# Kernel tuning notes

Hardware: AMD Instinct MI355X
Metric: run time of the kernel (lower is better)

## Reference

```python
import jax, jax.numpy as jnp
import numpy as np

NUM_CLASSES = 5
SMOOTH = 1e-5


def setup_inputs() -> dict:
    key = jax.random.key(0)
    k1, k2, k3 = jax.random.split(key, 3)
    B, C, X, Y, Z = 2, NUM_CLASSES, 128, 128, 128
    net_output = jax.random.normal(k1, (B, C, X, Y, Z), dtype=jnp.float32)
    target = jax.random.randint(k2, (B, 1, X, Y, Z), 0, C, dtype=jnp.int64)
    dist = jax.random.uniform(k3, (B, 1, X, Y, Z), dtype=jnp.float32)
    return {"net_output": net_output, "target": target, "dist": dist}


def reference(net_output, target, dist):
    # --- Distance-map penalized multi-class Dice ---
    p = jax.nn.softmax(net_output, axis=1)  # (B,C,X,Y,Z)
    gt = target[:, 0]  # (B,X,Y,Z)
    classes = jnp.arange(NUM_CLASSES)[None, :, None, None, None]
    y_onehot = (gt[:, None] == classes).astype(p.dtype)  # (B,C,X,Y,Z)
    # per-class, per-batch sums over spatial dims
    tp = jnp.sum(p * y_onehot * dist, axis=(2, 3, 4))  # (B,C), dist broadcasts over C
    denom = jnp.sum(p, axis=(2, 3, 4)) + jnp.sum(y_onehot, axis=(2, 3, 4))  # (B,C)
    dc = (2.0 * tp + SMOOTH) / (denom + SMOOTH)  # (B,C)
    # sum over classes of batch-mean, divided by num_classes == overall mean
    dpdc_loss = -jnp.mean(dc)
    # --- Cross entropy (mean over all voxels), target squeezed to class idx ---
    logp = jax.nn.log_softmax(net_output, axis=1)  # (B,C,X,Y,Z)
    nll = -jnp.take_along_axis(logp, target, axis=1)  # (B,1,X,Y,Z)
    ce_loss = jnp.mean(nll)
    # aggregate == 'sum', weight_ce = weight_dice = 1
    return ce_loss + dpdc_loss
```

## Files before the change

### kernel.cpp

```cpp
#include <hip/hip_runtime.h>

#define NC 5
#define NB 2
#define SPATIAL (128*128*128)
#define NVEC (SPATIAL/4)
#define SMOOTHF 1e-5f
#define NREP 32
#define GRIDX 1024
#define ITERS (NVEC / (GRIDX * 256))


__global__ __launch_bounds__(1024) void init_and_detect(
    const unsigned long long* __restrict__ t, float* __restrict__ acc) {
    acc[threadIdx.x] = 0.f;
    if (threadIdx.x == 0) {
        int is64 = 1;
        for (int i = 0; i < 64; ++i)
            if (t[i] >= 5ull) { is64 = 0; break; }
        ((int*)acc)[NREP * 32] = is64;
    }
}

__global__ __launch_bounds__(256) void dpdc_main(
    const float* __restrict__ net, const void* __restrict__ targ,
    const float* __restrict__ dist, float* __restrict__ acc)
{
    const int b = blockIdx.y;
    const int t64 = ((const int*)acc)[NREP * 32];
    const float4* nb = (const float4*)(net + (size_t)b * NC * SPATIAL);
    const float4* db = (const float4*)(dist + (size_t)b * SPATIAL);
    const int4* t32p = (const int4*)((const int*)targ + (size_t)b * SPATIAL);
    const ulonglong2* t64p =
        (const ulonglong2*)((const unsigned long long*)targ + (size_t)b * SPATIAL);

    float tp[NC] = {0,0,0,0,0}, sp[NC] = {0,0,0,0,0}, cnt[NC] = {0,0,0,0,0};
    float nll = 0.f;

    int i = blockIdx.x * blockDim.x + threadIdx.x;
    const int stride = GRIDX * 256;
    #pragma unroll
    for (int it = 0; it < ITERS; ++it, i += stride) {
        float4 l[NC];
        #pragma unroll
        for (int c = 0; c < NC; ++c) l[c] = nb[(size_t)c * NVEC + i];
        float4 dd = db[i];
        int tt[4];
        if (t64) {
            ulonglong2 a = t64p[2 * i];
            ulonglong2 bq = t64p[2 * i + 1];
            tt[0] = (int)a.x; tt[1] = (int)a.y;
            tt[2] = (int)bq.x; tt[3] = (int)bq.y;
        } else {
            int4 a = t32p[i];
            tt[0] = a.x; tt[1] = a.y; tt[2] = a.z; tt[3] = a.w;
        }
        const float* dv = (const float*)&dd;
        #pragma unroll
        for (int j = 0; j < 4; ++j) {
            float lc[NC];
            #pragma unroll
            for (int c = 0; c < NC; ++c) lc[c] = ((const float*)&l[c])[j];
            float m = fmaxf(fmaxf(fmaxf(lc[0], lc[1]), fmaxf(lc[2], lc[3])), lc[4]);
            float e[NC];
            float s = 0.f;
            #pragma unroll
            for (int c = 0; c < NC; ++c) { e[c] = __expf(lc[c] - m); s += e[c]; }
            float inv = 1.0f / s;
            int t = tt[j];
            float lsel = lc[4];
            #pragma unroll
            for (int c = 0; c < 4; ++c) lsel = (t == c) ? lc[c] : lsel;
            float pd = dv[j] * inv;
            #pragma unroll
            for (int c = 0; c < NC; ++c) {
                float p = e[c] * inv;
                sp[c] += p;
                tp[c] += (t == c) ? e[c] * pd : 0.f;
                cnt[c] += (t == c) ? 1.f : 0.f;
            }
            nll += __logf(s) - (lsel - m);
        }
    }

    __shared__ float red[4][16];
    float vals[16];
    #pragma unroll
    for (int c = 0; c < NC; ++c) {
        vals[c] = tp[c]; vals[5 + c] = sp[c]; vals[10 + c] = cnt[c];
    }
    vals[15] = nll;
    const int lane = threadIdx.x & 63;
    const int wave = threadIdx.x >> 6;
    #pragma unroll
    for (int k = 0; k < 16; ++k) {
        float v = vals[k];
        #pragma unroll
        for (int off = 32; off > 0; off >>= 1) v += __shfl_down(v, off, 64);
        if (lane == 0) red[wave][k] = v;
    }
    __syncthreads();
    if (threadIdx.x < 16) {
        int k = threadIdx.x;
        float v = red[0][k] + red[1][k] + red[2][k] + red[3][k];
        float* racc = acc + (blockIdx.x & (NREP - 1)) * 32;
        float* dst;
        if (k < 5)       dst = &racc[b * NC + k];
        else if (k < 10) dst = &racc[10 + b * NC + (k - 5)];
        else if (k < 15) dst = &racc[20 + b * NC + (k - 10)];
        else             dst = &racc[30];
        atomicAdd(dst, v);
    }
}

__global__ __launch_bounds__(64) void finalize(const float* __restrict__ acc,
                                               float* __restrict__ out) {
    __shared__ float red[31];
    int j = threadIdx.x;
    if (j < 31) {
        float s = 0.f;
        for (int r = 0; r < NREP; ++r) s += acc[r * 32 + j];
        red[j] = s;
    }
    __syncthreads();
    if (j == 0) {
        float dcsum = 0.f;
        for (int b = 0; b < NB; ++b)
            for (int c = 0; c < NC; ++c) {
                float tpv = red[b * NC + c];
                float spv = red[10 + b * NC + c];
                float cv  = red[20 + b * NC + c];
                dcsum += (2.f * tpv + SMOOTHF) / (spv + cv + SMOOTHF);
            }
        float ce = red[30] / (float)((size_t)NB * SPATIAL);
        out[0] = ce - dcsum / (float)(NB * NC);
    }
}

extern "C" void kernel_launch(void* const* d_in, const int* in_sizes, int n_in,
                              void* d_out, int out_size, void* d_ws, size_t ws_size,
                              hipStream_t stream) {
    const float* net  = (const float*)d_in[0];
    const void*  targ = d_in[1];
    const float* dist = (const float*)d_in[2];
    float* acc = (float*)d_ws;

    init_and_detect<<<1, 1024, 0, stream>>>(
        (const unsigned long long*)targ, acc);
    dim3 grid(GRIDX, NB);
    dpdc_main<<<grid, 256, 0, stream>>>(net, targ, dist, acc);
    finalize<<<1, 64, 0, stream>>>(acc, (float*)d_out);
}
```

Before: 37.25 us.

## Fuse finalize into main kernel via last-block counter and double grid

```diff
diff --git a/kernel.cpp b/kernel.cpp
--- a/kernel.cpp
+++ b/kernel.cpp
@@ -6,8 +6,8 @@
 #define NVEC (SPATIAL/4)
 #define SMOOTHF 1e-5f
 #define NREP 32
-#define GRIDX 1024
-#define ITERS (NVEC / (GRIDX * 256))
+#define GRIDX 2048
+#define TOTAL_BLOCKS (GRIDX * NB)
 
 
 __global__ __launch_bounds__(1024) void init_and_detect(
@@ -18,12 +18,14 @@
         for (int i = 0; i < 64; ++i)
             if (t[i] >= 5ull) { is64 = 0; break; }
         ((int*)acc)[NREP * 32] = is64;
+        ((int*)acc)[NREP * 32 + 1] = 0;
     }
 }
 
 __global__ __launch_bounds__(256) void dpdc_main(
     const float* __restrict__ net, const void* __restrict__ targ,
-    const float* __restrict__ dist, float* __restrict__ acc)
+    const float* __restrict__ dist, float* __restrict__ acc,
+    float* __restrict__ out)
 {
     const int b = blockIdx.y;
     const int t64 = ((const int*)acc)[NREP * 32];
@@ -33,13 +35,13 @@
     const ulonglong2* t64p =
         (const ulonglong2*)((const unsigned long long*)targ + (size_t)b * SPATIAL);
 
-    float tp[NC] = {0,0,0,0,0}, sp[NC] = {0,0,0,0,0}, cnt[NC] = {0,0,0,0,0};
+    float tp[NC], sp[NC], cnt[NC];
+    #pragma unroll
+    for (int c = 0; c < NC; ++c) { tp[c] = 0.f; sp[c] = 0.f; cnt[c] = 0.f; }
     float nll = 0.f;
 
-    int i = blockIdx.x * blockDim.x + threadIdx.x;
-    const int stride = GRIDX * 256;
-    #pragma unroll
-    for (int it = 0; it < ITERS; ++it, i += stride) {
+    const int i = blockIdx.x * 256 + threadIdx.x;
+    {
         float4 l[NC];
         #pragma unroll
         for (int c = 0; c < NC; ++c) l[c] = nb[(size_t)c * NVEC + i];
@@ -110,29 +112,41 @@
         else             dst = &racc[30];
         atomicAdd(dst, v);
     }
-}
 
-__global__ __launch_bounds__(64) void finalize(const float* __restrict__ acc,
-                                               float* __restrict__ out) {
-    __shared__ float red[31];
-    int j = threadIdx.x;
-    if (j < 31) {
-        float s = 0.f;
-        for (int r = 0; r < NREP; ++r) s += acc[r * 32 + j];
-        red[j] = s;
+    __shared__ int is_last;
+    __syncthreads();
+    if (threadIdx.x == 0) {
+        __threadfence();
+        int* done = (int*)acc + NREP * 32 + 1;
+        int old = atomicAdd(done, 1);
+        is_last = (old == TOTAL_BLOCKS - 1) ? 1 : 0;
     }
     __syncthreads();
-    if (j == 0) {
-        float dcsum = 0.f;
-        for (int b = 0; b < NB; ++b)
-            for (int c = 0; c < NC; ++c) {
-                float tpv = red[b * NC + c];
-                float spv = red[10 + b * NC + c];
-                float cv  = red[20 + b * NC + c];
-                dcsum += (2.f * tpv + SMOOTHF) / (spv + cv + SMOOTHF);
-            }
-        float ce = red[30] / (float)((size_t)NB * SPATIAL);
-        out[0] = ce - dcsum / (float)(NB * NC);
+    if (is_last) {
+        __shared__ float tot[31];
+        if (threadIdx.x == 0) __threadfence();
+        __syncthreads();
+        if (threadIdx.x < 31) {
+            float s = 0.f;
+            for (int r = 0; r < NREP; ++r)
+                s += __hip_atomic_load(&acc[r * 32 + threadIdx.x],
+                                       __ATOMIC_RELAXED,
+                                       __HIP_MEMORY_SCOPE_AGENT);
+            tot[threadIdx.x] = s;
+        }
+        __syncthreads();
+        if (threadIdx.x == 0) {
+            float dcsum = 0.f;
+            for (int bb = 0; bb < NB; ++bb)
+                for (int c = 0; c < NC; ++c) {
+                    float tpv = tot[bb * NC + c];
+                    float spv = tot[10 + bb * NC + c];
+                    float cv  = tot[20 + bb * NC + c];
+                    dcsum += (2.f * tpv + SMOOTHF) / (spv + cv + SMOOTHF);
+                }
+            float ce = tot[30] / (float)((size_t)NB * SPATIAL);
+            out[0] = ce - dcsum / (float)(NB * NC);
+        }
     }
 }
 
@@ -147,6 +161,5 @@
     init_and_detect<<<1, 1024, 0, stream>>>(
         (const unsigned long long*)targ, acc);
     dim3 grid(GRIDX, NB);
-    dpdc_main<<<grid, 256, 0, stream>>>(net, targ, dist, acc);
-    finalize<<<1, 64, 0, stream>>>(acc, (float*)d_out);
+    dpdc_main<<<grid, 256, 0, stream>>>(net, targ, dist, acc, (float*)d_out);
 }
```

Result: slower. 129.6 us (+247.9%).
